# Kernel tuning notes

Hardware: AMD Instinct MI355X
Metric: run time of the kernel (lower is better)

Reference implementation:

```python
import jax, jax.numpy as jnp
import numpy as np

# Multi-scale deformable attention core (Deformable DETR MSDeformAttn)
SHAPES = [(180, 180), (90, 90), (45, 45), (23, 23)]  # BEV pyramid; 180*180=32400 matches src slice
LEN = sum(h * w for h, w in SHAPES)  # 43054
D_MODEL, N_HEADS, N_LEVELS, N_POINTS = 256, 8, 4, 4
D_HEAD = D_MODEL // N_HEADS


def setup_inputs() -> dict:
    key = jax.random.key(0)
    ks = jax.random.split(key, 11)
    B = 1
    s = 0.02
    return {
        "query": jax.random.normal(ks[0], (B, LEN, D_MODEL), jnp.float32),
        "value_in": jax.random.normal(ks[1], (B, LEN, D_MODEL), jnp.float32),
        "reference_points": jax.random.uniform(ks[2], (B, LEN, N_LEVELS, 2), jnp.float32),
        "Wv": s * jax.random.normal(ks[3], (D_MODEL, D_MODEL), jnp.float32),
        "bv": jnp.zeros((D_MODEL,), jnp.float32),
        "Ws": s * jax.random.normal(ks[4], (D_MODEL, N_HEADS * N_LEVELS * N_POINTS * 2), jnp.float32),
        "bs": jnp.zeros((N_HEADS * N_LEVELS * N_POINTS * 2,), jnp.float32),
        "Wa": s * jax.random.normal(ks[5], (D_MODEL, N_HEADS * N_LEVELS * N_POINTS), jnp.float32),
        "ba": jnp.zeros((N_HEADS * N_LEVELS * N_POINTS,), jnp.float32),
        "Wo": s * jax.random.normal(ks[6], (D_MODEL, D_MODEL), jnp.float32),
        "bo": jnp.zeros((D_MODEL,), jnp.float32),
    }


def _sample_level(v, loc, Hl, Wl):
    """Bilinear sample (align_corners=False, zero padding) like F.grid_sample.
    v: [B, Hh, Hl*Wl, dh]; loc: [B, Lq, Hh, P, 2] normalized to [0,1].
    Returns [B, Hh, Lq, P, dh]."""
    B, Hh, N, dh = v.shape
    Lq, P = loc.shape[1], loc.shape[3]
    x = loc[..., 0] * Wl - 0.5
    y = loc[..., 1] * Hl - 0.5
    x0 = jnp.floor(x)
    y0 = jnp.floor(y)
    dx = x - x0
    dy = y - y0
    x0i = x0.astype(jnp.int32)
    y0i = y0.astype(jnp.int32)

    def tr(w):  # [B,Lq,Hh,P] -> [B,Hh,Lq,P]
        return jnp.transpose(w, (0, 2, 1, 3))

    def gather(ix, iy):
        valid = ((ix >= 0) & (ix < Wl) & (iy >= 0) & (iy < Hl)).astype(v.dtype)
        idx = jnp.clip(iy, 0, Hl - 1) * Wl + jnp.clip(ix, 0, Wl - 1)  # [B,Lq,Hh,P]
        idx_t = jnp.transpose(idx, (0, 2, 1, 3)).reshape(B, Hh, Lq * P)
        g = jnp.take_along_axis(v, idx_t[..., None], axis=2).reshape(B, Hh, Lq, P, dh)
        return g * tr(valid)[..., None]

    out = (gather(x0i, y0i) * tr((1 - dx) * (1 - dy))[..., None]
           + gather(x0i + 1, y0i) * tr(dx * (1 - dy))[..., None]
           + gather(x0i, y0i + 1) * tr((1 - dx) * dy)[..., None]
           + gather(x0i + 1, y0i + 1) * tr(dx * dy)[..., None])
    return out


def reference(query, value_in, reference_points, Wv, bv, Ws, bs, Wa, ba, Wo, bo):
    B, Lq, _ = query.shape
    # value projection -> [B, Len, Hh, dh]
    value = (value_in @ Wv + bv).reshape(B, LEN, N_HEADS, D_HEAD)
    # sampling offsets [B,Lq,Hh,L,P,2]
    offsets = (query @ Ws + bs).reshape(B, Lq, N_HEADS, N_LEVELS, N_POINTS, 2)
    # attention weights, softmax over L*P
    attn = jax.nn.softmax((query @ Wa + ba).reshape(B, Lq, N_HEADS, N_LEVELS * N_POINTS), axis=-1)
    attn = attn.reshape(B, Lq, N_HEADS, N_LEVELS, N_POINTS)
    # normalized sampling locations
    normalizer = jnp.array([[w, h] for h, w in SHAPES], jnp.float32)  # [L,2] as (W,H)
    loc = (reference_points[:, :, None, :, None, :]
           + offsets / normalizer[None, None, None, :, None, :])  # [B,Lq,Hh,L,P,2]

    acc = jnp.zeros((B, N_HEADS, Lq, D_HEAD), query.dtype)
    start = 0
    for lvl, (Hl, Wl) in enumerate(SHAPES):
        v = jnp.transpose(value[:, start:start + Hl * Wl], (0, 2, 1, 3))  # [B,Hh,N,dh]
        samp = _sample_level(v, loc[:, :, :, lvl], Hl, Wl)  # [B,Hh,Lq,P,dh]
        w = jnp.transpose(attn[:, :, :, lvl], (0, 2, 1, 3))  # [B,Hh,Lq,P]
        acc = acc + jnp.sum(samp * w[..., None], axis=3)
        start += Hl * Wl
    out = jnp.transpose(acc, (0, 2, 1, 3)).reshape(B, Lq, D_MODEL)
    return out @ Wo + bo
```

## Files before the change

kernel.cpp:

```cpp
#include <hip/hip_runtime.h>
#include <hip/hip_bf16.h>
#include <cstddef>

#define QLEN 43054

typedef __attribute__((ext_vector_type(8))) short short8;
typedef __attribute__((ext_vector_type(8))) unsigned short ushort8;
typedef __attribute__((ext_vector_type(4))) float f32x4;

__device__ __forceinline__ unsigned short f32_to_bf16_rne(float f) {
    unsigned int u = __float_as_uint(f);
    unsigned int r = (u + 0x7fffu + ((u >> 16) & 1u)) >> 16;
    return (unsigned short)r;
}
__device__ __forceinline__ float bf16_to_f32(unsigned short h) {
    return __uint_as_float(((unsigned int)h) << 16);
}

__global__ __launch_bounds__(256) void w_split(
    const float* __restrict__ W, unsigned short* __restrict__ hi,
    unsigned short* __restrict__ lo, int N)
{
    const int t = blockIdx.x * 256 + threadIdx.x;
    const int n = t >> 8;
    const int k = t & 255;
    const float w = W[(size_t)k * N + n];
    const unsigned short h = f32_to_bf16_rne(w);
    const float rem = w - bf16_to_f32(h);
    hi[(size_t)n * 256 + k] = h;
    lo[(size_t)n * 256 + k] = f32_to_bf16_rne(rem);
}

__global__ __launch_bounds__(256) void cvt_bf16(
    const float* __restrict__ in, unsigned short* __restrict__ out, int n4)
{
    int i = blockIdx.x * 256 + threadIdx.x;
    const int stride = gridDim.x * 256;
    for (; i < n4; i += stride) {
        const float4 v = ((const float4*)in)[i];
        ushort4 o;
        o.x = f32_to_bf16_rne(v.x);
        o.y = f32_to_bf16_rne(v.y);
        o.z = f32_to_bf16_rne(v.z);
        o.w = f32_to_bf16_rne(v.w);
        ((ushort4*)out)[i] = o;
    }
}

__global__ __launch_bounds__(256) void gemm_mfma(
    const unsigned short* __restrict__ A,
    const unsigned short* __restrict__ Bh,
    const unsigned short* __restrict__ Bl,
    const float* __restrict__ bias,
    float* __restrict__ Cf, unsigned short* __restrict__ Cb,
    int M, int N, int mode)
{
    const int lane = threadIdx.x & 63;
    const int w = threadIdx.x >> 6;
    const int wm = (w >> 1) * 64;
    const int wn = (w & 1) * 64;
    const int bm = blockIdx.x * 128;
    const int bn = blockIdx.y * 128;
    const int lr = lane & 15;
    const int lk = (lane >> 4) * 8;

    const unsigned short* aptr[4];
    const unsigned short* bhptr[4];
    const unsigned short* blptr[4];
    #pragma unroll
    for (int f = 0; f < 4; ++f) {
        int row = bm + wm + f * 16 + lr;
        row = min(row, M - 1);
        aptr[f] = A + (size_t)row * 256 + lk;
        const int col = bn + wn + f * 16 + lr;
        bhptr[f] = Bh + (size_t)col * 256 + lk;
        blptr[f] = Bl + (size_t)col * 256 + lk;
    }

    f32x4 acc[4][4];
    #pragma unroll
    for (int i = 0; i < 4; ++i)
        #pragma unroll
        for (int j = 0; j < 4; ++j)
            acc[i][j] = (f32x4){0.f, 0.f, 0.f, 0.f};

    #pragma unroll 2
    for (int k0 = 0; k0 < 256; k0 += 32) {
        short8 a[4], bh[4], bl[4];
        #pragma unroll
        for (int f = 0; f < 4; ++f) {
            a[f]  = *(const short8*)(aptr[f] + k0);
            bh[f] = *(const short8*)(bhptr[f] + k0);
            bl[f] = *(const short8*)(blptr[f] + k0);
        }
        #pragma unroll
        for (int i = 0; i < 4; ++i)
            #pragma unroll
            for (int j = 0; j < 4; ++j) {
                acc[i][j] = __builtin_amdgcn_mfma_f32_16x16x32_bf16(a[i], bh[j], acc[i][j], 0, 0, 0);
                acc[i][j] = __builtin_amdgcn_mfma_f32_16x16x32_bf16(a[i], bl[j], acc[i][j], 0, 0, 0);
            }
    }

    float bv[4];
    #pragma unroll
    for (int j = 0; j < 4; ++j) bv[j] = bias[bn + wn + j * 16 + lr];

    const int rbase = bm + wm + (lane >> 4) * 4;
    if (mode == 0) {
        #pragma unroll
        for (int i = 0; i < 4; ++i)
            #pragma unroll
            for (int r = 0; r < 4; ++r) {
                const int row = rbase + i * 16 + r;
                if (row < M) {
                    #pragma unroll
                    for (int j = 0; j < 4; ++j) {
                        const int col = bn + wn + j * 16 + lr;
                        Cf[(size_t)row * N + col] = acc[i][j][r] + bv[j];
                    }
                }
            }
    } else {
        #pragma unroll
        for (int i = 0; i < 4; ++i)
            #pragma unroll
            for (int r = 0; r < 4; ++r) {
                const int row = rbase + i * 16 + r;
                if (row < M) {
                    #pragma unroll
                    for (int j = 0; j < 4; ++j) {
                        const int col = bn + wn + j * 16 + lr;
                        Cb[(size_t)row * 256 + col] = f32_to_bf16_rne(acc[i][j][r] + bv[j]);
                    }
                }
            }
    }
}

__global__ __launch_bounds__(256) void msda_sample(
    const unsigned short* __restrict__ value,
    const float* __restrict__ offs,
    const float* __restrict__ attl,
    const float* __restrict__ refp,
    unsigned short* __restrict__ tmp)
{
    const int wv = (blockIdx.x << 2) + (threadIdx.x >> 6);
    const int lane = threadIdx.x & 63;
    const int q = wv >> 3;
    const int h = wv & 7;
    if (q >= QLEN) return;

    const int g = lane >> 2;
    const int j = lane & 3;

    const float offv  = offs[(size_t)q * 256 + h * 32 + (lane & 31)];
    const float logit = attl[(size_t)q * 128 + h * 16 + (lane & 15)];
    const float refv  = refp[(size_t)q * 8 + (lane & 7)];

    float mx = logit;
    #pragma unroll
    for (int msk = 1; msk < 16; msk <<= 1) mx = fmaxf(mx, __shfl_xor(mx, msk));
    const float e = __expf(logit - mx);
    float sm = e;
    #pragma unroll
    for (int msk = 1; msk < 16; msk <<= 1) sm += __shfl_xor(sm, msk);
    const float attw = e / sm;

    const int lvl = g >> 2;
    const int LW = (lvl == 0) ? 180 : (lvl == 1) ? 90 : (lvl == 2) ? 45 : 23;
    const int LS = (lvl == 0) ? 0 : (lvl == 1) ? 32400 : (lvl == 2) ? 40500 : 42525;

    const float ox = __shfl(offv, g * 2);
    const float oy = __shfl(offv, g * 2 + 1);
    const float aw = __shfl(attw, g);
    const float rx = __shfl(refv, lvl * 2);
    const float ry = __shfl(refv, lvl * 2 + 1);

    const float fLW = (float)LW;
    const float x = fmaf(rx, fLW, ox) - 0.5f;
    const float y = fmaf(ry, fLW, oy) - 0.5f;
    const float x0f = floorf(x), y0f = floorf(y);
    const float dx = x - x0f, dy = y - y0f;
    const int x0 = (int)x0f, y0 = (int)y0f;
    const int x1 = x0 + 1, y1 = y0 + 1;

    const bool vx0 = (x0 >= 0) && (x0 < LW);
    const bool vx1 = (x1 >= 0) && (x1 < LW);
    const bool vy0 = (y0 >= 0) && (y0 < LW);
    const bool vy1 = (y1 >= 0) && (y1 < LW);

    const int x0c = min(max(x0, 0), LW - 1);
    const int x1c = min(max(x1, 0), LW - 1);
    const int y0c = min(max(y0, 0), LW - 1);
    const int y1c = min(max(y1, 0), LW - 1);

    const float wx0 = 1.f - dx, wy0 = 1.f - dy;
    float w00 = wx0 * wy0 * aw;
    float w10 = dx  * wy0 * aw;
    float w01 = wx0 * dy  * aw;
    float w11 = dx  * dy  * aw;
    w00 = (vx0 && vy0) ? w00 : 0.f;
    w10 = (vx1 && vy0) ? w10 : 0.f;
    w01 = (vx0 && vy1) ? w01 : 0.f;
    w11 = (vx1 && vy1) ? w11 : 0.f;

    const unsigned short* __restrict__ vb = value + h * 32 + j * 8;
    const int r0 = LS + y0c * LW;
    const int r1 = LS + y1c * LW;
    const ushort8 v00 = *(const ushort8*)(vb + (size_t)(r0 + x0c) * 256);
    const ushort8 v10 = *(const ushort8*)(vb + (size_t)(r0 + x1c) * 256);
    const ushort8 v01 = *(const ushort8*)(vb + (size_t)(r1 + x0c) * 256);
    const ushort8 v11 = *(const ushort8*)(vb + (size_t)(r1 + x1c) * 256);

    float acc[8];
    #pragma unroll
    for (int e = 0; e < 8; ++e) {
        float s = w00 * bf16_to_f32(v00[e]);
        s = fmaf(w10, bf16_to_f32(v10[e]), s);
        s = fmaf(w01, bf16_to_f32(v01[e]), s);
        s = fmaf(w11, bf16_to_f32(v11[e]), s);
        acc[e] = s;
    }

    #pragma unroll
    for (int msk = 4; msk <= 32; msk <<= 1)
        #pragma unroll
        for (int e = 0; e < 8; ++e)
            acc[e] += __shfl_xor(acc[e], msk);

    if (g == 0) {
        ushort8 o;
        #pragma unroll
        for (int e = 0; e < 8; ++e) o[e] = f32_to_bf16_rne(acc[e]);
        *(ushort8*)(tmp + (size_t)q * 256 + h * 32 + j * 8) = o;
    }
}

extern "C" void kernel_launch(void* const* d_in, const int* in_sizes, int n_in,
                              void* d_out, int out_size, void* d_ws, size_t ws_size,
                              hipStream_t stream)
{
    const float* query    = (const float*)d_in[0];
    const float* value_in = (const float*)d_in[1];
    const float* refp     = (const float*)d_in[2];
    const float* Wv = (const float*)d_in[3];
    const float* bv = (const float*)d_in[4];
    const float* Ws = (const float*)d_in[5];
    const float* bs = (const float*)d_in[6];
    const float* Wa = (const float*)d_in[7];
    const float* ba = (const float*)d_in[8];
    const float* Wo = (const float*)d_in[9];
    const float* bo = (const float*)d_in[10];
    float* out = (float*)d_out;

    char* p = (char*)d_ws;
    const size_t SZ_BF = (size_t)QLEN * 256 * 2;
    unsigned short* q_bf   = (unsigned short*)p;               p += SZ_BF;
    unsigned short* vin_bf = (unsigned short*)p;               p += SZ_BF;
    unsigned short* val_bf = (unsigned short*)p;               p += SZ_BF;
    float*          offs   = (float*)p;                        p += (size_t)QLEN * 256 * 4;
    float*          attl   = (float*)p;                        p += (size_t)QLEN * 128 * 4;
    unsigned short* wtv_h  = (unsigned short*)p;               p += 256 * 256 * 2;
    unsigned short* wtv_l  = (unsigned short*)p;               p += 256 * 256 * 2;
    unsigned short* wts_h  = (unsigned short*)p;               p += 256 * 256 * 2;
    unsigned short* wts_l  = (unsigned short*)p;               p += 256 * 256 * 2;
    unsigned short* wta_h  = (unsigned short*)p;               p += 128 * 256 * 2;
    unsigned short* wta_l  = (unsigned short*)p;               p += 128 * 256 * 2;
    unsigned short* wto_h  = (unsigned short*)p;               p += 256 * 256 * 2;
    unsigned short* wto_l  = (unsigned short*)p;               p += 256 * 256 * 2;
    unsigned short* tmp_bf = vin_bf;

    const dim3 blk(256);
    const int MT = (QLEN + 127) / 128;
    const int n4 = QLEN * 256 / 4;

    w_split<<<256, blk, 0, stream>>>(Wv, wtv_h, wtv_l, 256);
    w_split<<<256, blk, 0, stream>>>(Ws, wts_h, wts_l, 256);
    w_split<<<128, blk, 0, stream>>>(Wa, wta_h, wta_l, 128);
    w_split<<<256, blk, 0, stream>>>(Wo, wto_h, wto_l, 256);
    cvt_bf16<<<1024, blk, 0, stream>>>(query,    q_bf,   n4);
    cvt_bf16<<<1024, blk, 0, stream>>>(value_in, vin_bf, n4);

    gemm_mfma<<<dim3(MT, 2), blk, 0, stream>>>(vin_bf, wtv_h, wtv_l, bv,
                                               nullptr, val_bf, QLEN, 256, 1);
    gemm_mfma<<<dim3(MT, 2), blk, 0, stream>>>(q_bf, wts_h, wts_l, bs,
                                               offs, nullptr, QLEN, 256, 0);
    gemm_mfma<<<dim3(MT, 1), blk, 0, stream>>>(q_bf, wta_h, wta_l, ba,
                                               attl, nullptr, QLEN, 128, 0);

    const int nwaves = QLEN * 8;
    msda_sample<<<dim3((nwaves + 3) / 4), blk, 0, stream>>>(val_bf, offs, attl, refp, tmp_bf);

    gemm_mfma<<<dim3(MT, 2), blk, 0, stream>>>(tmp_bf, wto_h, wto_l, bo,
                                               out, nullptr, QLEN, 256, 0);
}
```

Baseline: 464.9 us.

## Stage GEMM tiles in LDS via direct global-to-LDS loads with XOR swizzle

The GEMM kernel now loads each 128x32 K-slice of A and both weight halves into shared memory using global_load_lds, with an XOR swizzle to avoid bank conflicts. Waves then read their MFMA fragments from LDS instead of each wave loading its own fragments straight from global memory. This cuts redundant global/L2 traffic, since A rows and B columns are shared across the wave grid. The cost is two block barriers per K step and no double buffering, so load latency is not overlapped with compute.

Result: faster. 411.7 us (-11.4%).

```diff
diff --git a/kernel.cpp b/kernel.cpp
--- a/kernel.cpp
+++ b/kernel.cpp
@@ -47,7 +47,7 @@
     }
 }
 
-__global__ __launch_bounds__(256) void gemm_mfma(
+__global__ __launch_bounds__(256) void gemm_mfma_lds(
     const unsigned short* __restrict__ A,
     const unsigned short* __restrict__ Bh,
     const unsigned short* __restrict__ Bl,
@@ -55,27 +55,23 @@
     float* __restrict__ Cf, unsigned short* __restrict__ Cb,
     int M, int N, int mode)
 {
-    const int lane = threadIdx.x & 63;
-    const int w = threadIdx.x >> 6;
+    __shared__ alignas(16) unsigned short As[128 * 32];
+    __shared__ alignas(16) unsigned short Bhs[128 * 32];
+    __shared__ alignas(16) unsigned short Bls[128 * 32];
+
+    const int tid = threadIdx.x;
+    const int lane = tid & 63;
+    const int w = tid >> 6;
     const int wm = (w >> 1) * 64;
     const int wn = (w & 1) * 64;
     const int bm = blockIdx.x * 128;
     const int bn = blockIdx.y * 128;
-    const int lr = lane & 15;
-    const int lk = (lane >> 4) * 8;
-
-    const unsigned short* aptr[4];
-    const unsigned short* bhptr[4];
-    const unsigned short* blptr[4];
-    #pragma unroll
-    for (int f = 0; f < 4; ++f) {
-        int row = bm + wm + f * 16 + lr;
-        row = min(row, M - 1);
-        aptr[f] = A + (size_t)row * 256 + lk;
-        const int col = bn + wn + f * 16 + lr;
-        bhptr[f] = Bh + (size_t)col * 256 + lk;
-        blptr[f] = Bl + (size_t)col * 256 + lk;
-    }
+
+    const int rl = lane >> 2;
+    const int cd = lane & 3;
+
+    const int fr = lane & 15;
+    const int fc = lane >> 4;
 
     f32x4 acc[4][4];
     #pragma unroll
@@ -84,29 +80,54 @@
         for (int j = 0; j < 4; ++j)
             acc[i][j] = (f32x4){0.f, 0.f, 0.f, 0.f};
 
-    #pragma unroll 2
     for (int k0 = 0; k0 < 256; k0 += 32) {
-        short8 a[4], bh[4], bl[4];
+        #pragma unroll
+        for (int i = 0; i < 2; ++i) {
+            const int ii = w * 2 + i;
+            const int row = ii * 16 + rl;
+            const int cs = cd ^ ((row >> 1) & 3);
+            const size_t gof = (size_t)(k0 + cs * 8);
+            const int ra = min(bm + row, M - 1);
+            const int rb = bn + row;
+            __builtin_amdgcn_global_load_lds(
+                (const unsigned int*)(A + (size_t)ra * 256 + gof),
+                (unsigned int*)&As[ii * 512], 16, 0, 0);
+            __builtin_amdgcn_global_load_lds(
+                (const unsigned int*)(Bh + (size_t)rb * 256 + gof),
+                (unsigned int*)&Bhs[ii * 512], 16, 0, 0);
+            __builtin_amdgcn_global_load_lds(
+                (const unsigned int*)(Bl + (size_t)rb * 256 + gof),
+                (unsigned int*)&Bls[ii * 512], 16, 0, 0);
+        }
+        __syncthreads();
+
+        short8 a[4], bh4[4], bl4[4];
         #pragma unroll
         for (int f = 0; f < 4; ++f) {
-            a[f]  = *(const short8*)(aptr[f] + k0);
-            bh[f] = *(const short8*)(bhptr[f] + k0);
-            bl[f] = *(const short8*)(blptr[f] + k0);
+            const int rowA = wm + f * 16 + fr;
+            const int pcA = fc ^ ((rowA >> 1) & 3);
+            a[f] = *(const short8*)&As[rowA * 32 + pcA * 8];
+            const int rowB = wn + f * 16 + fr;
+            const int pcB = fc ^ ((rowB >> 1) & 3);
+            bh4[f] = *(const short8*)&Bhs[rowB * 32 + pcB * 8];
+            bl4[f] = *(const short8*)&Bls[rowB * 32 + pcB * 8];
         }
+
         #pragma unroll
         for (int i = 0; i < 4; ++i)
             #pragma unroll
             for (int j = 0; j < 4; ++j) {
-                acc[i][j] = __builtin_amdgcn_mfma_f32_16x16x32_bf16(a[i], bh[j], acc[i][j], 0, 0, 0);
-                acc[i][j] = __builtin_amdgcn_mfma_f32_16x16x32_bf16(a[i], bl[j], acc[i][j], 0, 0, 0);
+                acc[i][j] = __builtin_amdgcn_mfma_f32_16x16x32_bf16(a[i], bh4[j], acc[i][j], 0, 0, 0);
+                acc[i][j] = __builtin_amdgcn_mfma_f32_16x16x32_bf16(a[i], bl4[j], acc[i][j], 0, 0, 0);
             }
+        __syncthreads();
     }
 
     float bv[4];
     #pragma unroll
-    for (int j = 0; j < 4; ++j) bv[j] = bias[bn + wn + j * 16 + lr];
-
-    const int rbase = bm + wm + (lane >> 4) * 4;
+    for (int j = 0; j < 4; ++j) bv[j] = bias[bn + wn + j * 16 + fr];
+
+    const int rbase = bm + wm + fc * 4;
     if (mode == 0) {
         #pragma unroll
         for (int i = 0; i < 4; ++i)
@@ -116,7 +137,7 @@
                 if (row < M) {
                     #pragma unroll
                     for (int j = 0; j < 4; ++j) {
-                        const int col = bn + wn + j * 16 + lr;
+                        const int col = bn + wn + j * 16 + fr;
                         Cf[(size_t)row * N + col] = acc[i][j][r] + bv[j];
                     }
                 }
@@ -130,7 +151,7 @@
                 if (row < M) {
                     #pragma unroll
                     for (int j = 0; j < 4; ++j) {
-                        const int col = bn + wn + j * 16 + lr;
+                        const int col = bn + wn + j * 16 + fr;
                         Cb[(size_t)row * 256 + col] = f32_to_bf16_rne(acc[i][j][r] + bv[j]);
                     }
                 }
@@ -215,24 +236,24 @@
 
     float acc[8];
     #pragma unroll
-    for (int e = 0; e < 8; ++e) {
-        float s = w00 * bf16_to_f32(v00[e]);
-        s = fmaf(w10, bf16_to_f32(v10[e]), s);
-        s = fmaf(w01, bf16_to_f32(v01[e]), s);
-        s = fmaf(w11, bf16_to_f32(v11[e]), s);
-        acc[e] = s;
+    for (int e2 = 0; e2 < 8; ++e2) {
+        float s = w00 * bf16_to_f32(v00[e2]);
+        s = fmaf(w10, bf16_to_f32(v10[e2]), s);
+        s = fmaf(w01, bf16_to_f32(v01[e2]), s);
+        s = fmaf(w11, bf16_to_f32(v11[e2]), s);
+        acc[e2] = s;
     }
 
     #pragma unroll
     for (int msk = 4; msk <= 32; msk <<= 1)
         #pragma unroll
-        for (int e = 0; e < 8; ++e)
-            acc[e] += __shfl_xor(acc[e], msk);
+        for (int e2 = 0; e2 < 8; ++e2)
+            acc[e2] += __shfl_xor(acc[e2], msk);
 
     if (g == 0) {
         ushort8 o;
         #pragma unroll
-        for (int e = 0; e < 8; ++e) o[e] = f32_to_bf16_rne(acc[e]);
+        for (int e2 = 0; e2 < 8; ++e2) o[e2] = f32_to_bf16_rne(acc[e2]);
         *(ushort8*)(tmp + (size_t)q * 256 + h * 32 + j * 8) = o;
     }
 }
@@ -282,16 +303,16 @@
     cvt_bf16<<<1024, blk, 0, stream>>>(query,    q_bf,   n4);
     cvt_bf16<<<1024, blk, 0, stream>>>(value_in, vin_bf, n4);
 
-    gemm_mfma<<<dim3(MT, 2), blk, 0, stream>>>(vin_bf, wtv_h, wtv_l, bv,
-                                               nullptr, val_bf, QLEN, 256, 1);
-    gemm_mfma<<<dim3(MT, 2), blk, 0, stream>>>(q_bf, wts_h, wts_l, bs,
-                                               offs, nullptr, QLEN, 256, 0);
-    gemm_mfma<<<dim3(MT, 1), blk, 0, stream>>>(q_bf, wta_h, wta_l, ba,
-                                               attl, nullptr, QLEN, 128, 0);
+    gemm_mfma_lds<<<dim3(MT, 2), blk, 0, stream>>>(vin_bf, wtv_h, wtv_l, bv,
+                                                   nullptr, val_bf, QLEN, 256, 1);
+    gemm_mfma_lds<<<dim3(MT, 2), blk, 0, stream>>>(q_bf, wts_h, wts_l, bs,
+                                                   offs, nullptr, QLEN, 256, 0);
+    gemm_mfma_lds<<<dim3(MT, 1), blk, 0, stream>>>(q_bf, wta_h, wta_l, ba,
+                                                   attl, nullptr, QLEN, 128, 0);
 
     const int nwaves = QLEN * 8;
     msda_sample<<<dim3((nwaves + 3) / 4), blk, 0, stream>>>(val_bf, offs, attl, refp, tmp_bf);
 
-    gemm_mfma<<<dim3(MT, 2), blk, 0, stream>>>(tmp_bf, wto_h, wto_l, bo,
-                                               out, nullptr, QLEN, 256, 0);
-}
+    gemm_mfma_lds<<<dim3(MT, 2), blk, 0, stream>>>(tmp_bf, wto_h, wto_l, bo,
+                                                   out, nullptr, QLEN, 256, 0);
+}
```
